# Optimization experiments

Hardware: AMD Instinct MI355X
Metric: run time of the kernel (lower is better)

The kernel has to match this reference:

```python
import jax, jax.numpy as jnp
import numpy as np

MAX_LEN = 1024

def _lin(x, W, b=None):
    y = x @ W.T
    return y if b is None else y + b

def setup_inputs() -> dict:
    key = jax.random.key(0)
    ks = jax.random.split(key, 16)
    s = 0.05
    inp = {
        "x": jax.random.normal(ks[0], (8, 1024, 16), jnp.float32),
        "WQ": jax.random.normal(ks[1], (64, 16), jnp.float32) * s,
        "WK": jax.random.normal(ks[2], (64, 16), jnp.float32) * s,
        "VW1": jax.random.normal(ks[3], (16, 16), jnp.float32) * s,
        "Vb1": jnp.zeros((16,), jnp.float32),
        "VW2": jax.random.normal(ks[4], (16, 16), jnp.float32) * s,
        "Vb2": jnp.zeros((16,), jnp.float32),
        "VW3": jax.random.normal(ks[5], (8, 16), jnp.float32) * s,
        "Vb3": jnp.zeros((8,), jnp.float32),
        "PW1": jax.random.normal(ks[6], (64, 1), jnp.float32) * s,
        "Pb1": jnp.zeros((64,), jnp.float32),
        "PW2": jax.random.normal(ks[7], (64, 64), jnp.float32) * s,
        "Pb2": jnp.zeros((64,), jnp.float32),
        "PW3": jax.random.normal(ks[8], (64, 64), jnp.float32) * s,
        "Pb3": jnp.zeros((64,), jnp.float32),
        "PW4": jax.random.normal(ks[9], (32, 64), jnp.float32) * s,
        "Pb4": jnp.zeros((32,), jnp.float32),
        "offset": jnp.array([-10.0], jnp.float32),
        "HW1": jax.random.normal(ks[10], (256, 256), jnp.float32) * s,
        "Hb1": jnp.zeros((256,), jnp.float32),
        "HW2": jax.random.normal(ks[11], (256, 256), jnp.float32) * s,
        "Hb2": jnp.zeros((256,), jnp.float32),
        "HW3": jax.random.normal(ks[12], (4, 256), jnp.float32) * s,
        "Hb3": jnp.zeros((4,), jnp.float32),
    }
    return inp

def reference(x, WQ, WK, VW1, Vb1, VW2, Vb2, VW3, Vb3,
              PW1, Pb1, PW2, Pb2, PW3, Pb3, PW4, Pb4,
              offset, HW1, Hb1, HW2, Hb2, HW3, Hb3):
    B, L, _ = x.shape
    # Q/K projections and raw scores  [B, L, L]
    q = _lin(x, WQ)
    k = _lin(x, WK)
    a = jnp.einsum('bik,bjk->bij', q, k)
    d_k = q.shape[-1]
    # sigmoid attention with zeroed diagonal
    Iinf = 1.0 - jnp.eye(L, dtype=x.dtype)
    attention = jax.nn.sigmoid(a / jnp.sqrt(jnp.asarray(d_k, x.dtype)) + offset[0]) * Iinf
    # parametric set function: Phi MLP over t in [0,1]
    t = jnp.linspace(0.0, 1.0, MAX_LEN, dtype=x.dtype)[:L, None]  # [L, 1]
    h = jax.nn.relu(_lin(t, PW1, Pb1))
    h = jax.nn.relu(_lin(h, PW2, Pb2))
    h = jax.nn.relu(_lin(h, PW3, Pb3))
    SetPhi = _lin(h, PW4, Pb4)  # [L, set_dim]
    # relative-position gather: SetPhi[|i-j|] -> [L, L, set_dim]
    ar = jnp.arange(L)
    Tidx = jnp.abs(ar[:, None] - ar[None, :])
    rel = SetPhi[Tidx]
    set_values = jnp.einsum('bij,ijk->bik', attention, rel)  # [B, L, set_dim]
    # V MLP with sigmoid output  [B, L, vdim]
    v = jax.nn.relu(_lin(x, VW1, Vb1))
    v = jax.nn.relu(_lin(v, VW2, Vb2))
    v = jax.nn.sigmoid(_lin(v, VW3, Vb3))
    summarized = jnp.einsum('bij,bik->bjk', set_values, v)  # [B, set_dim, vdim]
    # head MLP + softmax (num_classes > 1)
    flat = summarized.reshape(B, -1)
    h = jax.nn.relu(_lin(flat, HW1, Hb1))
    h = jax.nn.relu(_lin(h, HW2, Hb2))
    return jax.nn.softmax(_lin(h, HW3, Hb3), axis=-1)
```

## Files before the change

kernel.cpp:

```cpp
#include <hip/hip_runtime.h>
#include <hip/hip_bf16.h>


#define LSEQ 1024
#define DK   64
#define EMB  16
#define VDIM 8

typedef __attribute__((ext_vector_type(8))) short bf16x8;
typedef __attribute__((ext_vector_type(4))) float f32x4;

__device__ __forceinline__ unsigned short f2bf(float f) {
  union { float f; unsigned u; } v; v.f = f;
  unsigned r = v.u + 0x7fffu + ((v.u >> 16) & 1u);
  return (unsigned short)(r >> 16);
}

__device__ __forceinline__ f32x4 mfma16(bf16x8 a, bf16x8 b, f32x4 c) {
  return __builtin_amdgcn_mfma_f32_16x16x32_bf16(a, b, c, 0, 0, 0);
}

__global__ __launch_bounds__(256) void prep_kernel(
    const float* __restrict__ x,  const float* __restrict__ WQ,  const float* __restrict__ WK,
    const float* __restrict__ VW1, const float* __restrict__ Vb1,
    const float* __restrict__ VW2, const float* __restrict__ Vb2,
    const float* __restrict__ VW3, const float* __restrict__ Vb3,
    const float* __restrict__ PW1, const float* __restrict__ Pb1,
    const float* __restrict__ PW2, const float* __restrict__ Pb2,
    const float* __restrict__ PW3, const float* __restrict__ Pb3,
    const float* __restrict__ PW4, const float* __restrict__ Pb4,
    unsigned short* __restrict__ qb, unsigned short* __restrict__ kb,
    unsigned short* __restrict__ phiT, float* __restrict__ vws,
    float* __restrict__ summar)
{
  __shared__ float s1[272];
  __shared__ float s2[272];
  int bid = blockIdx.x, tid = threadIdx.x;

  if (bid < 4096) {
    int g = bid * 256 + tid;
    int row = g >> 7, c = g & 127;
    const float* xr = x + row * EMB;
    const float* wr = ((c < 64) ? WQ : WK) + (c & 63) * EMB;
    float acc = 0.f;
    #pragma unroll
    for (int e = 0; e < 4; ++e) {
      f32x4 xv = *(const f32x4*)(xr + e * 4);
      f32x4 wv = *(const f32x4*)(wr + e * 4);
      acc += xv[0]*wv[0] + xv[1]*wv[1] + xv[2]*wv[2] + xv[3]*wv[3];
    }
    unsigned short* dst = (c < 64) ? qb : kb;
    dst[row * DK + (c & 63)] = f2bf(acc);

  } else if (bid < 4608) {
    int lb = bid - 4096;
    int r = tid >> 4, cc = tid & 15;
    int row = lb * 16 + r;
    const float* xr = x + row * EMB;
    float acc = Vb1[cc];
    #pragma unroll
    for (int e4 = 0; e4 < 4; ++e4) {
      f32x4 wv = *(const f32x4*)(VW1 + cc * 16 + e4 * 4);
      acc += xr[e4*4+0]*wv[0] + xr[e4*4+1]*wv[1] + xr[e4*4+2]*wv[2] + xr[e4*4+3]*wv[3];
    }
    s1[r * 17 + cc] = fmaxf(acc, 0.f);
    __syncthreads();
    acc = Vb2[cc];
    #pragma unroll
    for (int e4 = 0; e4 < 4; ++e4) {
      f32x4 wv = *(const f32x4*)(VW2 + cc * 16 + e4 * 4);
      acc += s1[r*17+e4*4+0]*wv[0] + s1[r*17+e4*4+1]*wv[1] + s1[r*17+e4*4+2]*wv[2] + s1[r*17+e4*4+3]*wv[3];
    }
    s2[r * 17 + cc] = fmaxf(acc, 0.f);
    __syncthreads();
    if (cc < 8) {
      acc = Vb3[cc];
      #pragma unroll
      for (int e4 = 0; e4 < 4; ++e4) {
        f32x4 wv = *(const f32x4*)(VW3 + cc * 16 + e4 * 4);
        acc += s2[r*17+e4*4+0]*wv[0] + s2[r*17+e4*4+1]*wv[1] + s2[r*17+e4*4+2]*wv[2] + s2[r*17+e4*4+3]*wv[3];
      }
      vws[row * VDIM + cc] = 1.f / (1.f + __expf(-acc));
    }

  } else if (bid < 4864) {
    int lb = bid - 4608;
    int r = tid >> 6, cc = tid & 63;
    int row = lb * 4 + r;
    float t = (float)row * (1.0f / 1023.0f);
    s1[r * 65 + cc] = fmaxf(PW1[cc] * t + Pb1[cc], 0.f);
    __syncthreads();
    float acc = Pb2[cc];
    #pragma unroll
    for (int e4 = 0; e4 < 16; ++e4) {
      f32x4 wv = *(const f32x4*)(PW2 + cc * 64 + e4 * 4);
      acc += s1[r*65+e4*4+0]*wv[0] + s1[r*65+e4*4+1]*wv[1] + s1[r*65+e4*4+2]*wv[2] + s1[r*65+e4*4+3]*wv[3];
    }
    s2[r * 65 + cc] = fmaxf(acc, 0.f);
    __syncthreads();
    acc = Pb3[cc];
    #pragma unroll
    for (int e4 = 0; e4 < 16; ++e4) {
      f32x4 wv = *(const f32x4*)(PW3 + cc * 64 + e4 * 4);
      acc += s2[r*65+e4*4+0]*wv[0] + s2[r*65+e4*4+1]*wv[1] + s2[r*65+e4*4+2]*wv[2] + s2[r*65+e4*4+3]*wv[3];
    }
    s1[r * 65 + cc] = fmaxf(acc, 0.f);
    __syncthreads();
    if (cc < 32) {
      acc = Pb4[cc];
      #pragma unroll
      for (int e4 = 0; e4 < 16; ++e4) {
        f32x4 wv = *(const f32x4*)(PW4 + cc * 64 + e4 * 4);
        acc += s1[r*65+e4*4+0]*wv[0] + s1[r*65+e4*4+1]*wv[1] + s1[r*65+e4*4+2]*wv[2] + s1[r*65+e4*4+3]*wv[3];
      }
      phiT[cc * LSEQ + row] = f2bf(acc);
    }

  } else {
    int idx = (bid - 4864) * 256 + tid;
    summar[idx] = 0.f;
  }
}

__global__ __launch_bounds__(256) void attn_kernel(
    const unsigned short* __restrict__ qb, const unsigned short* __restrict__ kb,
    const unsigned short* __restrict__ phiT, const float* __restrict__ vws,
    const float* __restrict__ offs, float* __restrict__ summar)
{
  __shared__ float A2_s[16 * 1026];
  __shared__ float sv_w[4][16][17];
  __shared__ float v_s[16][8];

  int bid = blockIdx.x;
  int b  = bid >> 6;
  int i0 = (bid & 63) << 4;
  int tid = threadIdx.x;
  int lane = tid & 63, w = tid >> 6;
  int lr = lane & 15, lg = lane >> 4;

  for (int idx = tid; idx < 16 * 1026; idx += 256) A2_s[idx] = 0.f;
  if (tid < 128) v_s[tid >> 3][tid & 7] = vws[(b * LSEQ + i0 + (tid >> 3)) * VDIM + (tid & 7)];

  float off = offs[0];

  const unsigned short* qrow = qb + (size_t)(b * LSEQ + i0 + lr) * DK + lg * 8;
  bf16x8 afr0 = *(const bf16x8*)qrow;
  bf16x8 afr1 = *(const bf16x8*)(qrow + 32);

  const unsigned short* kbase = kb + (size_t)b * LSEQ * DK;
  int jbl = (w * 2) * 16;

  const unsigned short* kr = kbase + (jbl + lr) * DK + lg * 8;
  bf16x8 b00 = *(const bf16x8*)kr;
  bf16x8 b01 = *(const bf16x8*)(kr + 32);
  bf16x8 b10 = *(const bf16x8*)(kr + 16 * DK);
  bf16x8 b11 = *(const bf16x8*)(kr + 16 * DK + 32);

  __syncthreads();

  for (int t = 0; t < 8; ++t) {
    int j0 = t * 128;
    f32x4 acc0 = {0.f, 0.f, 0.f, 0.f}, acc1 = {0.f, 0.f, 0.f, 0.f};
    acc0 = mfma16(afr0, b00, acc0);
    acc0 = mfma16(afr1, b01, acc0);
    acc1 = mfma16(afr0, b10, acc1);
    acc1 = mfma16(afr1, b11, acc1);
    if (t < 7) {
      const unsigned short* kr2 = kbase + ((t + 1) * 128 + jbl + lr) * DK + lg * 8;
      b00 = *(const bf16x8*)kr2;
      b01 = *(const bf16x8*)(kr2 + 32);
      b10 = *(const bf16x8*)(kr2 + 16 * DK);
      b11 = *(const bf16x8*)(kr2 + 16 * DK + 32);
    }
    #pragma unroll
    for (int r2 = 0; r2 < 4; ++r2) {
      int row = 4 * lg + r2;
      int gi = i0 + row;
      int gj0 = j0 + jbl + lr;
      int gj1 = gj0 + 16;
      float s0 = (gi == gj0) ? 0.f : 1.f / (1.f + __expf(-(acc0[r2] * 0.125f + off)));
      float s1v = (gi == gj1) ? 0.f : 1.f / (1.f + __expf(-(acc1[r2] * 0.125f + off)));
      int d0 = gi - gj0; d0 = (d0 < 0) ? -d0 : d0;
      int d1 = gi - gj1; d1 = (d1 < 0) ? -d1 : d1;
      atomicAdd(&A2_s[row * 1026 + d0], s0);
      atomicAdd(&A2_s[row * 1026 + d1], s1v);
    }
  }
  __syncthreads();

  {
    int ct = w & 1, kh = w >> 1;
    f32x4 acc = {0.f, 0.f, 0.f, 0.f};
    const unsigned short* ph = phiT + (ct * 16 + lr) * LSEQ + kh * 512 + lg * 8;
    const float* arow = A2_s + lr * 1026 + kh * 512 + lg * 8;
    for (int s = 0; s < 16; ++s) {
      bf16x8 af;
      const float* ap = arow + s * 32;
      #pragma unroll
      for (int e = 0; e < 8; ++e) af[e] = (short)f2bf(ap[e]);
      bf16x8 bfv = *(const bf16x8*)(ph + s * 32);
      acc = mfma16(af, bfv, acc);
    }
    #pragma unroll
    for (int r2 = 0; r2 < 4; ++r2)
      sv_w[w][4 * lg + r2][lr] = acc[r2];
  }
  __syncthreads();

  {
    int sd = tid >> 3, kk = tid & 7;
    int ct = sd >> 4, cl = sd & 15;
    float a = 0.f;
    #pragma unroll
    for (int il = 0; il < 16; ++il)
      a += (sv_w[ct][il][cl] + sv_w[ct + 2][il][cl]) * v_s[il][kk];
    unsafeAtomicAdd(&summar[b * 256 + sd * 8 + kk], a);
  }
}

__global__ __launch_bounds__(1024) void head_kernel(
    const float* __restrict__ summar,
    const float* __restrict__ HW1, const float* __restrict__ Hb1,
    const float* __restrict__ HW2, const float* __restrict__ Hb2,
    const float* __restrict__ HW3, const float* __restrict__ Hb3,
    float* __restrict__ out)
{
  __shared__ float fb[256];
  __shared__ float part[4][260];
  __shared__ float lgt[4];
  int b = blockIdx.x, tid = threadIdx.x;
  int c = tid & 255, qt = tid >> 8;

  if (qt == 0) fb[c] = summar[b * 256 + c];
  __syncthreads();
  {
    const float* wr = HW1 + c * 256 + qt * 64;
    const float* xr = fb + qt * 64;
    float a = 0.f;
    #pragma unroll
    for (int e = 0; e < 16; ++e) {
      f32x4 wv = *(const f32x4*)(wr + e * 4);
      f32x4 xv = *(const f32x4*)(xr + e * 4);
      a += wv[0]*xv[0] + wv[1]*xv[1] + wv[2]*xv[2] + wv[3]*xv[3];
    }
    part[qt][c] = a;
  }
  __syncthreads();
  if (qt == 0)
    fb[c] = fmaxf(part[0][c] + part[1][c] + part[2][c] + part[3][c] + Hb1[c], 0.f);
  __syncthreads();
  {
    const float* wr = HW2 + c * 256 + qt * 64;
    const float* xr = fb + qt * 64;
    float a = 0.f;
    #pragma unroll
    for (int e = 0; e < 16; ++e) {
      f32x4 wv = *(const f32x4*)(wr + e * 4);
      f32x4 xv = *(const f32x4*)(xr + e * 4);
      a += wv[0]*xv[0] + wv[1]*xv[1] + wv[2]*xv[2] + wv[3]*xv[3];
    }
    part[qt][c] = a;
  }
  __syncthreads();
  if (qt == 0)
    fb[c] = fmaxf(part[0][c] + part[1][c] + part[2][c] + part[3][c] + Hb2[c], 0.f);
  __syncthreads();
  if (tid < 4) {
    float a = Hb3[tid];
    for (int e = 0; e < 256; ++e) a += fb[e] * HW3[tid * 256 + e];
    lgt[tid] = a;
  }
  __syncthreads();
  if (tid == 0) {
    float m = fmaxf(fmaxf(lgt[0], lgt[1]), fmaxf(lgt[2], lgt[3]));
    float e0 = __expf(lgt[0] - m), e1 = __expf(lgt[1] - m);
    float e2 = __expf(lgt[2] - m), e3 = __expf(lgt[3] - m);
    float s = e0 + e1 + e2 + e3;
    out[b * 4 + 0] = e0 / s;
    out[b * 4 + 1] = e1 / s;
    out[b * 4 + 2] = e2 / s;
    out[b * 4 + 3] = e3 / s;
  }
}

extern "C" void kernel_launch(void* const* d_in, const int* in_sizes, int n_in,
                              void* d_out, int out_size, void* d_ws, size_t ws_size,
                              hipStream_t stream)
{
  const float* x   = (const float*)d_in[0];
  const float* WQ  = (const float*)d_in[1];
  const float* WK  = (const float*)d_in[2];
  const float* VW1 = (const float*)d_in[3];
  const float* Vb1 = (const float*)d_in[4];
  const float* VW2 = (const float*)d_in[5];
  const float* Vb2 = (const float*)d_in[6];
  const float* VW3 = (const float*)d_in[7];
  const float* Vb3 = (const float*)d_in[8];
  const float* PW1 = (const float*)d_in[9];
  const float* Pb1 = (const float*)d_in[10];
  const float* PW2 = (const float*)d_in[11];
  const float* Pb2 = (const float*)d_in[12];
  const float* PW3 = (const float*)d_in[13];
  const float* Pb3 = (const float*)d_in[14];
  const float* PW4 = (const float*)d_in[15];
  const float* Pb4 = (const float*)d_in[16];
  const float* offs= (const float*)d_in[17];
  const float* HW1 = (const float*)d_in[18];
  const float* Hb1 = (const float*)d_in[19];
  const float* HW2 = (const float*)d_in[20];
  const float* Hb2 = (const float*)d_in[21];
  const float* HW3 = (const float*)d_in[22];
  const float* Hb3 = (const float*)d_in[23];

  char* ws = (char*)d_ws;
  unsigned short* qb   = (unsigned short*)(ws);
  unsigned short* kb   = (unsigned short*)(ws + (1u << 20));
  unsigned short* phiT = (unsigned short*)(ws + (2u << 20));
  float* vws    = (float*)(ws + (2u << 20) + (1u << 16));
  float* summar = (float*)(ws + (2u << 20) + (1u << 16) + (1u << 18));

  prep_kernel<<<dim3(4872), dim3(256), 0, stream>>>(
      x, WQ, WK, VW1, Vb1, VW2, Vb2, VW3, Vb3,
      PW1, Pb1, PW2, Pb2, PW3, Pb3, PW4, Pb4,
      qb, kb, phiT, vws, summar);

  attn_kernel<<<dim3(512), dim3(256), 0, stream>>>(
      qb, kb, phiT, vws, offs, summar);

  head_kernel<<<dim3(8), dim3(1024), 0, stream>>>(
      summar, HW1, Hb1, HW2, Hb2, HW3, Hb3, (float*)d_out);
}
```

Before: 187.4 us.

## Double attention block threads and preload all K fragments in registers

Launches the attention kernel with 512 threads (8 waves) instead of 256. Each wave now covers a contiguous 128-column slab of keys and loads all eight K tile fragments up front in two batches, in place of the old one-tile-ahead prefetch loop. The phi contraction is split into quarter-ranges with phi fragments preloaded, and the shared-memory atomics switch to unsafeAtomicAdd. This is meant to raise parallelism and memory-level overlap per block, at the cost of more registers per thread and more waves contending on the same LDS accumulation rows.

```diff
diff --git a/kernel.cpp b/kernel.cpp
--- a/kernel.cpp
+++ b/kernel.cpp
@@ -122,13 +122,13 @@
   }
 }
 
-__global__ __launch_bounds__(256) void attn_kernel(
+__global__ __launch_bounds__(512, 4) void attn_kernel(
     const unsigned short* __restrict__ qb, const unsigned short* __restrict__ kb,
     const unsigned short* __restrict__ phiT, const float* __restrict__ vws,
     const float* __restrict__ offs, float* __restrict__ summar)
 {
   __shared__ float A2_s[16 * 1026];
-  __shared__ float sv_w[4][16][17];
+  __shared__ float sv_w[8][16][17];
   __shared__ float v_s[16][8];
 
   int bid = blockIdx.x;
@@ -138,7 +138,7 @@
   int lane = tid & 63, w = tid >> 6;
   int lr = lane & 15, lg = lane >> 4;
 
-  for (int idx = tid; idx < 16 * 1026; idx += 256) A2_s[idx] = 0.f;
+  for (int idx = tid; idx < 16 * 1026; idx += 512) A2_s[idx] = 0.f;
   if (tid < 128) v_s[tid >> 3][tid & 7] = vws[(b * LSEQ + i0 + (tid >> 3)) * VDIM + (tid & 7)];
 
   float off = offs[0];
@@ -147,59 +147,69 @@
   bf16x8 afr0 = *(const bf16x8*)qrow;
   bf16x8 afr1 = *(const bf16x8*)(qrow + 32);
 
-  const unsigned short* kbase = kb + (size_t)b * LSEQ * DK;
-  int jbl = (w * 2) * 16;
-
-  const unsigned short* kr = kbase + (jbl + lr) * DK + lg * 8;
-  bf16x8 b00 = *(const bf16x8*)kr;
-  bf16x8 b01 = *(const bf16x8*)(kr + 32);
-  bf16x8 b10 = *(const bf16x8*)(kr + 16 * DK);
-  bf16x8 b11 = *(const bf16x8*)(kr + 16 * DK + 32);
-
-  __syncthreads();
-
-  for (int t = 0; t < 8; ++t) {
-    int j0 = t * 128;
-    f32x4 acc0 = {0.f, 0.f, 0.f, 0.f}, acc1 = {0.f, 0.f, 0.f, 0.f};
-    acc0 = mfma16(afr0, b00, acc0);
-    acc0 = mfma16(afr1, b01, acc0);
-    acc1 = mfma16(afr0, b10, acc1);
-    acc1 = mfma16(afr1, b11, acc1);
-    if (t < 7) {
-      const unsigned short* kr2 = kbase + ((t + 1) * 128 + jbl + lr) * DK + lg * 8;
-      b00 = *(const bf16x8*)kr2;
-      b01 = *(const bf16x8*)(kr2 + 32);
-      b10 = *(const bf16x8*)(kr2 + 16 * DK);
-      b11 = *(const bf16x8*)(kr2 + 16 * DK + 32);
-    }
+  const unsigned short* kbase = kb + (size_t)b * LSEQ * DK + (size_t)(w * 128 + lr) * DK + lg * 8;
+  bf16x8 bk0[8], bk1[8];
+  #pragma unroll
+  for (int st = 0; st < 4; ++st) {
+    bk0[2*st]   = *(const bf16x8*)(kbase + st * 16 * DK);
+    bk0[2*st+1] = *(const bf16x8*)(kbase + st * 16 * DK + 32);
+  }
+
+  __syncthreads();
+
+  #pragma unroll
+  for (int st = 0; st < 4; ++st) {
+    bk1[2*st]   = *(const bf16x8*)(kbase + (st + 4) * 16 * DK);
+    bk1[2*st+1] = *(const bf16x8*)(kbase + (st + 4) * 16 * DK + 32);
+  }
+
+  #pragma unroll
+  for (int st = 0; st < 4; ++st) {
+    f32x4 acc = {0.f, 0.f, 0.f, 0.f};
+    acc = mfma16(afr0, bk0[2*st], acc);
+    acc = mfma16(afr1, bk0[2*st+1], acc);
     #pragma unroll
     for (int r2 = 0; r2 < 4; ++r2) {
       int row = 4 * lg + r2;
       int gi = i0 + row;
-      int gj0 = j0 + jbl + lr;
-      int gj1 = gj0 + 16;
-      float s0 = (gi == gj0) ? 0.f : 1.f / (1.f + __expf(-(acc0[r2] * 0.125f + off)));
-      float s1v = (gi == gj1) ? 0.f : 1.f / (1.f + __expf(-(acc1[r2] * 0.125f + off)));
-      int d0 = gi - gj0; d0 = (d0 < 0) ? -d0 : d0;
-      int d1 = gi - gj1; d1 = (d1 < 0) ? -d1 : d1;
-      atomicAdd(&A2_s[row * 1026 + d0], s0);
-      atomicAdd(&A2_s[row * 1026 + d1], s1v);
+      int gj = w * 128 + st * 16 + lr;
+      float s = (gi == gj) ? 0.f : 1.f / (1.f + __expf(-(acc[r2] * 0.125f + off)));
+      int d = gi - gj; d = (d < 0) ? -d : d;
+      unsafeAtomicAdd(&A2_s[row * 1026 + d], s);
+    }
+  }
+  #pragma unroll
+  for (int st = 0; st < 4; ++st) {
+    f32x4 acc = {0.f, 0.f, 0.f, 0.f};
+    acc = mfma16(afr0, bk1[2*st], acc);
+    acc = mfma16(afr1, bk1[2*st+1], acc);
+    #pragma unroll
+    for (int r2 = 0; r2 < 4; ++r2) {
+      int row = 4 * lg + r2;
+      int gi = i0 + row;
+      int gj = w * 128 + (st + 4) * 16 + lr;
+      float s = (gi == gj) ? 0.f : 1.f / (1.f + __expf(-(acc[r2] * 0.125f + off)));
+      int d = gi - gj; d = (d < 0) ? -d : d;
+      unsafeAtomicAdd(&A2_s[row * 1026 + d], s);
     }
   }
   __syncthreads();
 
   {
-    int ct = w & 1, kh = w >> 1;
+    int ct = w & 1, kq = w >> 1;
+    const unsigned short* ph = phiT + (ct * 16 + lr) * LSEQ + kq * 256 + lg * 8;
+    bf16x8 pf[8];
+    #pragma unroll
+    for (int s = 0; s < 8; ++s) pf[s] = *(const bf16x8*)(ph + s * 32);
+    const float* arow = A2_s + lr * 1026 + kq * 256 + lg * 8;
     f32x4 acc = {0.f, 0.f, 0.f, 0.f};
-    const unsigned short* ph = phiT + (ct * 16 + lr) * LSEQ + kh * 512 + lg * 8;
-    const float* arow = A2_s + lr * 1026 + kh * 512 + lg * 8;
-    for (int s = 0; s < 16; ++s) {
+    #pragma unroll
+    for (int s = 0; s < 8; ++s) {
       bf16x8 af;
       const float* ap = arow + s * 32;
       #pragma unroll
       for (int e = 0; e < 8; ++e) af[e] = (short)f2bf(ap[e]);
-      bf16x8 bfv = *(const bf16x8*)(ph + s * 32);
-      acc = mfma16(af, bfv, acc);
+      acc = mfma16(af, pf[s], acc);
     }
     #pragma unroll
     for (int r2 = 0; r2 < 4; ++r2)
@@ -207,13 +217,16 @@
   }
   __syncthreads();
 
-  {
+  if (tid < 256) {
     int sd = tid >> 3, kk = tid & 7;
     int ct = sd >> 4, cl = sd & 15;
     float a = 0.f;
     #pragma unroll
-    for (int il = 0; il < 16; ++il)
-      a += (sv_w[ct][il][cl] + sv_w[ct + 2][il][cl]) * v_s[il][kk];
+    for (int il = 0; il < 16; ++il) {
+      float sv = sv_w[ct][il][cl] + sv_w[ct + 2][il][cl]
+               + sv_w[ct + 4][il][cl] + sv_w[ct + 6][il][cl];
+      a += sv * v_s[il][kk];
+    }
     unsafeAtomicAdd(&summar[b * 256 + sd * 8 + kk], a);
   }
 }
@@ -324,7 +337,7 @@
       PW1, Pb1, PW2, Pb2, PW3, Pb3, PW4, Pb4,
       qb, kb, phiT, vws, summar);
 
-  attn_kernel<<<dim3(512), dim3(256), 0, stream>>>(
+  attn_kernel<<<dim3(512), dim3(512), 0, stream>>>(
       qb, kb, phiT, vws, offs, summar);
 
   head_kernel<<<dim3(8), dim3(1024), 0, stream>>>(
```

New measurement: 189.0 us. Within noise of the previous version (+0.9%).
